# Kernel tuning notes

Hardware: AMD Instinct MI355X
Metric: run time of the kernel (lower is better)

## Reference

```python
import jax, jax.numpy as jnp
import numpy as np

V = 100000   # vocab_size / n_nodes
D = 128      # embedding_dim
B = 16384    # batch of items
S = 64       # samples per item
E = 640000   # edges


def setup_inputs() -> dict:
    key = jax.random.key(0)
    k1, k2, k3, k4, k5 = jax.random.split(key, 5)
    items = jax.random.randint(k1, (B,), 0, V)
    samples = jax.random.randint(k2, (B, S), 0, V)
    edge_index = jax.random.randint(k3, (2, E), 0, V)
    # xavier_uniform for embedding table and GCN linear weight
    emb_lim = float(np.sqrt(6.0 / (V + D)))
    emb_weight = jax.random.uniform(k4, (V, D), minval=-emb_lim, maxval=emb_lim, dtype=jnp.float32)
    w_lim = float(np.sqrt(6.0 / (D + D)))
    gcn_weight = jax.random.uniform(k5, (D, D), minval=-w_lim, maxval=w_lim, dtype=jnp.float32)
    gcn_bias = jnp.zeros((D,), dtype=jnp.float32)
    return {"items": items, "samples": samples, "edge_index": edge_index,
            "emb_weight": emb_weight, "gcn_weight": gcn_weight, "gcn_bias": gcn_bias}


def gcn_conv(x, edge_index, W, b, num_nodes):
    """PyG GCNConv: add self-loops, symmetric D^-1/2 (A+I) D^-1/2 normalization,
    linear transform, scatter-add aggregation, bias."""
    h = x @ W  # [N, D]
    loops = jnp.arange(num_nodes)
    src = jnp.concatenate([edge_index[0], loops])  # source nodes j
    dst = jnp.concatenate([edge_index[1], loops])  # target nodes i
    deg = jax.ops.segment_sum(jnp.ones_like(src, dtype=h.dtype), dst, num_segments=num_nodes)
    deg_inv_sqrt = jnp.where(deg > 0, jax.lax.rsqrt(jnp.maximum(deg, 1.0)), 0.0)
    norm = deg_inv_sqrt[src] * deg_inv_sqrt[dst]  # [E+N]
    msgs = norm[:, None] * h[src]                  # gather-scale
    out = jax.ops.segment_sum(msgs, dst, num_segments=num_nodes)  # scatter-add
    return out + b


def reference(items, samples, edge_index, emb_weight, gcn_weight, gcn_bias):
    nodes = gcn_conv(emb_weight, edge_index, gcn_weight, gcn_bias, emb_weight.shape[0])  # [V, D]
    item_emb = nodes[items]      # [B, D]
    sample_emb = nodes[samples]  # [B, S, D]
    # bmm([B,1,D], [B,D,S]).squeeze(1) == einsum
    scores = jnp.einsum('bd,bsd->bs', item_emb, sample_emb)
    return scores
```

## Files before the change

kernel.cpp:

```cpp
#include <hip/hip_runtime.h>
#include <hip/hip_bf16.h>

#define V_NODES 100000
#define DIM 128
#define BATCH 16384
#define SAMP 64
#define NEDGE 640000
#define NSAMP (BATCH * SAMP)

__device__ __forceinline__ float bl(unsigned u) { return __uint_as_float(u << 16); }
__device__ __forceinline__ float bh(unsigned u) { return __uint_as_float(u & 0xffff0000u); }
__device__ __forceinline__ unsigned short f2bf(float x) {
    unsigned u = __float_as_uint(x);
    return (unsigned short)((u + 0x7fffu + ((u >> 16) & 1u)) >> 16);
}

typedef __attribute__((ext_vector_type(8))) short bf16x8;
typedef __attribute__((ext_vector_type(4))) float f32x4;

__global__ void k_count(const int* __restrict__ key, int* __restrict__ cnt, int E) {
    int e = blockIdx.x * blockDim.x + threadIdx.x;
    if (e < E) atomicAdd(&cnt[key[e]], 1);
}

__global__ void k_bsum(const int* __restrict__ cnt, int* __restrict__ bsum, int V) {
    __shared__ int red[4];
    int b = blockIdx.x, t = threadIdx.x;
    int s = 0;
    int base = b * 1024;
    for (int i = 0; i < 4; ++i) {
        int idx = base + i * 256 + t;
        if (idx < V) s += cnt[idx];
    }
    for (int m = 32; m >= 1; m >>= 1) s += __shfl_xor(s, m, 64);
    int lane = t & 63, wid = t >> 6;
    if (lane == 0) red[wid] = s;
    __syncthreads();
    if (t == 0) bsum[b] = red[0] + red[1] + red[2] + red[3];
}

__global__ void k_bscan(const int* __restrict__ bsum, int* __restrict__ boff, int nb) {
    int l = threadIdx.x;
    int i0 = 2 * l, i1 = 2 * l + 1;
    int v0 = (i0 < nb) ? bsum[i0] : 0;
    int v1 = (i1 < nb) ? bsum[i1] : 0;
    int s = v0 + v1;
    int x = s;
    for (int off = 1; off < 64; off <<= 1) {
        int n = __shfl_up(x, off, 64);
        if (l >= off) x += n;
    }
    int excl = x - s;
    if (i0 < nb) boff[i0] = excl;
    if (i1 < nb) boff[i1] = excl + v0;
}

__global__ void k_offs(const int* __restrict__ cnt, const int* __restrict__ boff,
                       int* __restrict__ offs, float* __restrict__ dinv,
                       int* __restrict__ cursor, int V) {
    __shared__ int wsum[4];
    int b = blockIdx.x, t = threadIdx.x;
    int lane = t & 63, wid = t >> 6;
    int base = b * 1024 + t * 4;
    int c[4];
    for (int j = 0; j < 4; ++j) {
        int idx = base + j;
        c[j] = (idx < V) ? cnt[idx] : 0;
    }
    int tot = c[0] + c[1] + c[2] + c[3];
    int x = tot;
    for (int off = 1; off < 64; off <<= 1) {
        int n = __shfl_up(x, off, 64);
        if (lane >= off) x += n;
    }
    int lex = x - tot;
    if (lane == 63) wsum[wid] = x;
    __syncthreads();
    int wpre = 0;
    for (int w = 0; w < wid; ++w) wpre += wsum[w];
    int o = boff[b] + wpre + lex;
    int pre = 0;
    for (int j = 0; j < 4; ++j) {
        int idx = base + j;
        if (idx < V) {
            int o0 = o + pre;
            offs[idx] = o0;
            cursor[idx] = o0;
            dinv[idx] = 1.0f / sqrtf((float)(c[j] + 1));
        }
        pre += c[j];
    }
}

__global__ void k_fill(const int* __restrict__ src, const int* __restrict__ dst,
                       int* __restrict__ cursor, int* __restrict__ csr, int E) {
    int e = blockIdx.x * blockDim.x + threadIdx.x;
    if (e < E) {
        int pos = atomicAdd(&cursor[dst[e]], 1);
        csr[pos] = src[e];
    }
}

#define WTP 136
__global__ __launch_bounds__(256) void k_hgemm(const float* __restrict__ emb,
                      unsigned short* __restrict__ h_bf,
                      const float* __restrict__ W, int V) {
    __shared__ unsigned short At[64][WTP];
    __shared__ unsigned short Wt[128][WTP];
    int t = threadIdx.x;
    int rowbase = blockIdx.x * 64;
    for (int i = t; i < 128 * 32; i += 256) {
        int k  = i >> 5;
        int n4 = (i & 31) << 2;
        float4 w4 = *(const float4*)(W + k * 128 + n4);
        Wt[n4 + 0][k] = f2bf(w4.x);
        Wt[n4 + 1][k] = f2bf(w4.y);
        Wt[n4 + 2][k] = f2bf(w4.z);
        Wt[n4 + 3][k] = f2bf(w4.w);
    }
    for (int i = t; i < 64 * 32; i += 256) {
        int r  = i >> 5;
        int c4 = (i & 31) << 2;
        int gr = rowbase + r;
        float4 a4 = (gr < V) ? *(const float4*)(emb + (size_t)gr * 128 + c4)
                             : make_float4(0.f, 0.f, 0.f, 0.f);
        ushort4 p;
        p.x = f2bf(a4.x); p.y = f2bf(a4.y); p.z = f2bf(a4.z); p.w = f2bf(a4.w);
        *(ushort4*)&At[r][c4] = p;
    }
    __syncthreads();
    int wid = t >> 6, lane = t & 63;
    int r16  = lane & 15;
    int kgrp = lane >> 4;
    f32x4 acc[8] = {};
    #pragma unroll
    for (int ks = 0; ks < 4; ++ks) {
        bf16x8 a = *(const bf16x8*)&At[wid * 16 + r16][ks * 32 + kgrp * 8];
        #pragma unroll
        for (int n = 0; n < 8; ++n) {
            bf16x8 b = *(const bf16x8*)&Wt[n * 16 + r16][ks * 32 + kgrp * 8];
            acc[n] = __builtin_amdgcn_mfma_f32_16x16x32_bf16(a, b, acc[n], 0, 0, 0);
        }
    }
    __syncthreads();
    #pragma unroll
    for (int n = 0; n < 8; ++n) {
        #pragma unroll
        for (int r = 0; r < 4; ++r) {
            At[wid * 16 + kgrp * 4 + r][n * 16 + r16] = f2bf(acc[n][r]);
        }
    }
    __syncthreads();
    for (int i = t; i < 64 * 16; i += 256) {
        int r  = i >> 4;
        int c8 = (i & 15) << 3;
        int gr = rowbase + r;
        if (gr < V) *(uint4*)(h_bf + (size_t)gr * 128 + c8) = *(const uint4*)&At[r][c8];
    }
}

__global__ __launch_bounds__(256) void k_agg(const unsigned short* __restrict__ h_bf,
                     const int* __restrict__ offs, const int* __restrict__ cnt,
                     const int* __restrict__ csr, const float* __restrict__ dinv,
                     const float* __restrict__ bias,
                     unsigned* __restrict__ nodes_h, int V) {
    int wid = threadIdx.x >> 6;
    int lane = threadIdx.x & 63;
    int v = blockIdx.x * 4 + wid;
    if (v >= V) return;
    float dv = dinv[v];
    int beg = offs[v], num = cnt[v];
    int nid = 0; float nw = 0.0f;
    if (lane < num) {
        nid = csr[beg + lane];
        nw = dinv[nid];
    }
    unsigned u0 = ((const unsigned*)(h_bf + (size_t)v * DIM))[lane];
    float wself = dv * dv;
    float2 bv = ((const float2*)bias)[lane];
    float ax = bv.x + wself * bl(u0), ay = bv.y + wself * bh(u0);
    float cx = 0.f, cy = 0.f;
    int n0 = min(num, 64);
    int i = 0;
    for (; i + 4 <= n0; i += 4) {
        int s0 = __shfl(nid, i,     64);
        int s1 = __shfl(nid, i + 1, 64);
        int s2 = __shfl(nid, i + 2, 64);
        int s3 = __shfl(nid, i + 3, 64);
        float w0 = dv * __shfl(nw, i,     64);
        float w1 = dv * __shfl(nw, i + 1, 64);
        float w2 = dv * __shfl(nw, i + 2, 64);
        float w3 = dv * __shfl(nw, i + 3, 64);
        unsigned e0 = ((const unsigned*)(h_bf + (size_t)s0 * DIM))[lane];
        unsigned e1 = ((const unsigned*)(h_bf + (size_t)s1 * DIM))[lane];
        unsigned e2 = ((const unsigned*)(h_bf + (size_t)s2 * DIM))[lane];
        unsigned e3 = ((const unsigned*)(h_bf + (size_t)s3 * DIM))[lane];
        ax += w0 * bl(e0); ay += w0 * bh(e0);
        cx += w1 * bl(e1); cy += w1 * bh(e1);
        ax += w2 * bl(e2); ay += w2 * bh(e2);
        cx += w3 * bl(e3); cy += w3 * bh(e3);
    }
    for (; i < n0; ++i) {
        int s = __shfl(nid, i, 64);
        float w = dv * __shfl(nw, i, 64);
        unsigned u = ((const unsigned*)(h_bf + (size_t)s * DIM))[lane];
        ax += w * bl(u); ay += w * bh(u);
    }
    for (int k = 64; k < num; ++k) {
        int s = csr[beg + k];
        float w = dv * dinv[s];
        unsigned u = ((const unsigned*)(h_bf + (size_t)s * DIM))[lane];
        ax += w * bl(u); ay += w * bh(u);
    }
    ax += cx; ay += cy;
    nodes_h[(size_t)v * (DIM / 2) + lane] =
        (unsigned)f2bf(ax) | ((unsigned)f2bf(ay) << 16);
}

__global__ __launch_bounds__(256) void k_score(const unsigned short* __restrict__ nodes_h,
                      const int* __restrict__ items, const int* __restrict__ samples,
                      float* __restrict__ out) {
    int b = blockIdx.x;
    int t = threadIdx.x;
    int q = t & 3;
    int sidx = t >> 2;
    int item = items[b];
    const uint4* irow = (const uint4*)(nodes_h + (size_t)item * DIM) + q * 4;
    uint4 a[4];
    #pragma unroll
    for (int c = 0; c < 4; ++c) a[c] = irow[c];

    int j = samples[b * SAMP + sidx];
    const uint4* srow = (const uint4*)(nodes_h + (size_t)j * DIM) + q * 4;
    uint4 s4[4];
    #pragma unroll
    for (int c = 0; c < 4; ++c) s4[c] = srow[c];

    float p = 0.f;
    #pragma unroll
    for (int c = 0; c < 4; ++c) {
        uint4 av = a[c], sv = s4[c];
        p += bl(av.x) * bl(sv.x) + bh(av.x) * bh(sv.x);
        p += bl(av.y) * bl(sv.y) + bh(av.y) * bh(sv.y);
        p += bl(av.z) * bl(sv.z) + bh(av.z) * bh(sv.z);
        p += bl(av.w) * bl(sv.w) + bh(av.w) * bh(sv.w);
    }
    p += __shfl_xor(p, 1, 64);
    p += __shfl_xor(p, 2, 64);
    if (q == 0) out[b * SAMP + sidx] = p;
}

extern "C" void kernel_launch(void* const* d_in, const int* in_sizes, int n_in,
                              void* d_out, int out_size, void* d_ws, size_t ws_size,
                              hipStream_t stream) {
    const int*   items   = (const int*)d_in[0];
    const int*   samples = (const int*)d_in[1];
    const int*   edges   = (const int*)d_in[2];
    const float* emb     = (const float*)d_in[3];
    const float* W       = (const float*)d_in[4];
    const float* bias    = (const float*)d_in[5];
    float* out = (float*)d_out;

    char* ws = (char*)d_ws;
    int*   cnt    = (int*)(ws + 0);
    int*   cursor = (int*)(ws + (512 << 10));
    float* dinv   = (float*)(ws + (1 << 20));
    int*   offs   = (int*)(ws + 3 * (512 << 10));
    int*   bsum   = (int*)(ws + (2 << 20));
    int*   boff   = (int*)(ws + (2 << 20) + (4 << 10));
    int*   csr    = (int*)(ws + (4 << 20));
    unsigned short* h_bf    = (unsigned short*)(ws + (8 << 20));
    unsigned*       nodes_h = (unsigned*)(ws + (34 << 20));

    const int* esrc = edges;
    const int* edst = edges + NEDGE;

    hipMemsetAsync(cnt, 0, V_NODES * sizeof(int), stream);

    int nb = (V_NODES + 1023) / 1024;
    k_count<<<(NEDGE + 255) / 256, 256, 0, stream>>>(edst, cnt, NEDGE);
    k_bsum <<<nb, 256, 0, stream>>>(cnt, bsum, V_NODES);
    k_bscan<<<1, 64, 0, stream>>>(bsum, boff, nb);
    k_offs <<<nb, 256, 0, stream>>>(cnt, boff, offs, dinv, cursor, V_NODES);
    k_fill <<<(NEDGE + 255) / 256, 256, 0, stream>>>(esrc, edst, cursor, csr, NEDGE);
    k_hgemm<<<(V_NODES + 63) / 64, 256, 0, stream>>>(emb, h_bf, W, V_NODES);
    k_agg  <<<(V_NODES + 3) / 4, 256, 0, stream>>>(h_bf, offs, cnt, csr, dinv, bias, nodes_h, V_NODES);
    k_score<<<BATCH, 256, 0, stream>>>((const unsigned short*)nodes_h, items, samples, out);
}
```

Before: 187.5 us.

## Pre-convert GCN weight to bf16 once and load A fragments directly from global

Adds a small kernel that transposes and converts W to bf16 once, so each GEMM block copies 32KB of ready bf16 into a single XOR-swizzled LDS buffer. Previously every block did fp32 loads and scalar transposed LDS stores. The A operand is now loaded straight from global into registers and converted in-register, which drops the A staging pass through LDS and shrinks LDS use. The hipMemsetAsync is replaced by a zeroing kernel. This adds two kernel launches and puts more register pressure on the GEMM.

```diff
diff --git a/kernel.cpp b/kernel.cpp
--- a/kernel.cpp
+++ b/kernel.cpp
@@ -17,6 +17,23 @@
 
 typedef __attribute__((ext_vector_type(8))) short bf16x8;
 typedef __attribute__((ext_vector_type(4))) float f32x4;
+
+__global__ void k_zero(int4* __restrict__ p, int n4) {
+    int i = blockIdx.x * blockDim.x + threadIdx.x;
+    if (i < n4) p[i] = make_int4(0, 0, 0, 0);
+}
+
+__global__ void k_wcvt(const float* __restrict__ W, unsigned short* __restrict__ wt_bf) {
+    int g = blockIdx.x * blockDim.x + threadIdx.x;
+    int n = g & 127;
+    int k4 = (g >> 7) << 2;
+    ushort4 o;
+    o.x = f2bf(W[(k4 + 0) * 128 + n]);
+    o.y = f2bf(W[(k4 + 1) * 128 + n]);
+    o.z = f2bf(W[(k4 + 2) * 128 + n]);
+    o.w = f2bf(W[(k4 + 3) * 128 + n]);
+    *(ushort4*)(wt_bf + n * 128 + k4) = o;
+}
 
 __global__ void k_count(const int* __restrict__ key, int* __restrict__ cnt, int E) {
     int e = blockIdx.x * blockDim.x + threadIdx.x;
@@ -101,44 +118,45 @@
     }
 }
 
-#define WTP 136
 __global__ __launch_bounds__(256) void k_hgemm(const float* __restrict__ emb,
                       unsigned short* __restrict__ h_bf,
-                      const float* __restrict__ W, int V) {
-    __shared__ unsigned short At[64][WTP];
-    __shared__ unsigned short Wt[128][WTP];
+                      const unsigned short* __restrict__ wt_bf, int V) {
+    __shared__ unsigned short WtL[128 * 128];
     int t = threadIdx.x;
     int rowbase = blockIdx.x * 64;
-    for (int i = t; i < 128 * 32; i += 256) {
-        int k  = i >> 5;
-        int n4 = (i & 31) << 2;
-        float4 w4 = *(const float4*)(W + k * 128 + n4);
-        Wt[n4 + 0][k] = f2bf(w4.x);
-        Wt[n4 + 1][k] = f2bf(w4.y);
-        Wt[n4 + 2][k] = f2bf(w4.z);
-        Wt[n4 + 3][k] = f2bf(w4.w);
-    }
-    for (int i = t; i < 64 * 32; i += 256) {
-        int r  = i >> 5;
-        int c4 = (i & 31) << 2;
-        int gr = rowbase + r;
-        float4 a4 = (gr < V) ? *(const float4*)(emb + (size_t)gr * 128 + c4)
-                             : make_float4(0.f, 0.f, 0.f, 0.f);
-        ushort4 p;
-        p.x = f2bf(a4.x); p.y = f2bf(a4.y); p.z = f2bf(a4.z); p.w = f2bf(a4.w);
-        *(ushort4*)&At[r][c4] = p;
-    }
-    __syncthreads();
+    for (int i = 0; i < 8; ++i) {
+        int j = t + i * 256;
+        int n = j >> 4, c8 = (j & 15) << 3;
+        uint4 v = *(const uint4*)(wt_bf + n * 128 + c8);
+        *(uint4*)&WtL[n * 128 + (c8 ^ ((n & 7) << 3))] = v;
+    }
     int wid = t >> 6, lane = t & 63;
     int r16  = lane & 15;
     int kgrp = lane >> 4;
+    int grow = rowbase + wid * 16 + r16;
+    const float* arow = emb + (size_t)grow * 128 + kgrp * 8;
+    bool ok = (grow < V);
+    float4 af[8];
+    #pragma unroll
+    for (int ks = 0; ks < 4; ++ks) {
+        af[2 * ks]     = ok ? *(const float4*)(arow + ks * 32)     : make_float4(0.f, 0.f, 0.f, 0.f);
+        af[2 * ks + 1] = ok ? *(const float4*)(arow + ks * 32 + 4) : make_float4(0.f, 0.f, 0.f, 0.f);
+    }
+    __syncthreads();
     f32x4 acc[8] = {};
     #pragma unroll
     for (int ks = 0; ks < 4; ++ks) {
-        bf16x8 a = *(const bf16x8*)&At[wid * 16 + r16][ks * 32 + kgrp * 8];
+        float4 a0 = af[2 * ks], a1 = af[2 * ks + 1];
+        bf16x8 a;
+        a[0] = (short)f2bf(a0.x); a[1] = (short)f2bf(a0.y);
+        a[2] = (short)f2bf(a0.z); a[3] = (short)f2bf(a0.w);
+        a[4] = (short)f2bf(a1.x); a[5] = (short)f2bf(a1.y);
+        a[6] = (short)f2bf(a1.z); a[7] = (short)f2bf(a1.w);
+        int kc = ks * 32 + kgrp * 8;
         #pragma unroll
         for (int n = 0; n < 8; ++n) {
-            bf16x8 b = *(const bf16x8*)&Wt[n * 16 + r16][ks * 32 + kgrp * 8];
+            int wr = n * 16 + r16;
+            bf16x8 b = *(const bf16x8*)&WtL[wr * 128 + (kc ^ ((wr & 7) << 3))];
             acc[n] = __builtin_amdgcn_mfma_f32_16x16x32_bf16(a, b, acc[n], 0, 0, 0);
         }
     }
@@ -147,15 +165,18 @@
     for (int n = 0; n < 8; ++n) {
         #pragma unroll
         for (int r = 0; r < 4; ++r) {
-            At[wid * 16 + kgrp * 4 + r][n * 16 + r16] = f2bf(acc[n][r]);
+            int drow = wid * 16 + kgrp * 4 + r;
+            int dcol = n * 16 + r16;
+            WtL[drow * 128 + (dcol ^ ((drow & 7) << 3))] = f2bf(acc[n][r]);
         }
     }
     __syncthreads();
-    for (int i = t; i < 64 * 16; i += 256) {
-        int r  = i >> 4;
-        int c8 = (i & 15) << 3;
+    for (int i = 0; i < 4; ++i) {
+        int j = t + i * 256;
+        int r = j >> 4, c8 = (j & 15) << 3;
+        uint4 v = *(const uint4*)&WtL[r * 128 + (c8 ^ ((r & 7) << 3))];
         int gr = rowbase + r;
-        if (gr < V) *(uint4*)(h_bf + (size_t)gr * 128 + c8) = *(const uint4*)&At[r][c8];
+        if (gr < V) *(uint4*)(h_bf + (size_t)gr * 128 + c8) = v;
     }
 }
 
@@ -268,6 +289,7 @@
     int*   offs   = (int*)(ws + 3 * (512 << 10));
     int*   bsum   = (int*)(ws + (2 << 20));
     int*   boff   = (int*)(ws + (2 << 20) + (4 << 10));
+    unsigned short* wt_bf = (unsigned short*)(ws + (3 << 20));
     int*   csr    = (int*)(ws + (4 << 20));
     unsigned short* h_bf    = (unsigned short*)(ws + (8 << 20));
     unsigned*       nodes_h = (unsigned*)(ws + (34 << 20));
@@ -275,15 +297,15 @@
     const int* esrc = edges;
     const int* edst = edges + NEDGE;
 
-    hipMemsetAsync(cnt, 0, V_NODES * sizeof(int), stream);
-
     int nb = (V_NODES + 1023) / 1024;
+    k_zero <<<98, 256, 0, stream>>>((int4*)cnt, V_NODES / 4);
+    k_wcvt <<<16, 256, 0, stream>>>(W, wt_bf);
     k_count<<<(NEDGE + 255) / 256, 256, 0, stream>>>(edst, cnt, NEDGE);
     k_bsum <<<nb, 256, 0, stream>>>(cnt, bsum, V_NODES);
     k_bscan<<<1, 64, 0, stream>>>(bsum, boff, nb);
     k_offs <<<nb, 256, 0, stream>>>(cnt, boff, offs, dinv, cursor, V_NODES);
     k_fill <<<(NEDGE + 255) / 256, 256, 0, stream>>>(esrc, edst, cursor, csr, NEDGE);
-    k_hgemm<<<(V_NODES + 63) / 64, 256, 0, stream>>>(emb, h_bf, W, V_NODES);
+    k_hgemm<<<(V_NODES + 63) / 64, 256, 0, stream>>>(emb, h_bf, wt_bf, V_NODES);
     k_agg  <<<(V_NODES + 3) / 4, 256, 0, stream>>>(h_bf, offs, cnt, csr, dinv, bias, nodes_h, V_NODES);
     k_score<<<BATCH, 256, 0, stream>>>((const unsigned short*)nodes_h, items, samples, out);
 }
```

Result: faster. 172.4 us (-8.0%).
